# Performance work log

Hardware: AMD Instinct MI355X
Metric: run time of the kernel (lower is better)

Reference implementation:

```python
import jax, jax.numpy as jnp
import numpy as np

B, N, K, DIN, DM, DOUT = 4, 4096, 16, 256, 256, 256


def setup_inputs() -> dict:
    key = jax.random.key(0)
    ks = jax.random.split(key, 14)
    s = lambda k, shape: (jax.random.normal(k, shape, jnp.float32) * 0.02)
    return dict(
        xyz=jax.random.normal(ks[0], (B, N, 3), jnp.float32),
        features=jax.random.normal(ks[1], (B, N, DIN), jnp.float32),
        fc_delta_w1=s(ks[2], (3, DM)), fc_delta_b1=jnp.zeros((DM,), jnp.float32),
        fc_delta_w2=s(ks[3], (DM, DM)), fc_delta_b2=jnp.zeros((DM,), jnp.float32),
        fc1_w=s(ks[4], (DIN, DM)), fc1_b=jnp.zeros((DM,), jnp.float32),
        wq=s(ks[5], (DM, DM)), wk=s(ks[6], (DM, DM)), wv=s(ks[7], (DM, DM)),
        fc_gamma_w1=s(ks[8], (DM, DM)), fc_gamma_b1=jnp.zeros((DM,), jnp.float32),
        fc_gamma_w2=s(ks[9], (DM, DM)), fc_gamma_b2=jnp.zeros((DM,), jnp.float32),
        fc2_w=s(ks[10], (DM, DOUT)), fc2_b=jnp.zeros((DOUT,), jnp.float32),
        sc_w=s(ks[11], (DIN, DOUT)), sc_b=jnp.zeros((DOUT,), jnp.float32),
    )


def reference(xyz, features, fc_delta_w1, fc_delta_b1, fc_delta_w2, fc_delta_b2,
              fc1_w, fc1_b, wq, wk, wv, fc_gamma_w1, fc_gamma_b1,
              fc_gamma_w2, fc_gamma_b2, fc2_w, fc2_b, sc_w, sc_b):
    # kNN via squared euclidean distances (same ordering as cdist topk)
    x2 = jnp.sum(xyz * xyz, axis=-1)                                   # (B,N)
    d2 = x2[:, :, None] + x2[:, None, :] - 2.0 * jnp.einsum('bnd,bmd->bnm', xyz, xyz)
    knn_idx = jax.lax.top_k(-d2, K)[1]                                 # (B,N,K)

    gather = jax.vmap(lambda a, i: a[i])                               # per-batch gather
    knn_xyz = gather(xyz, knn_idx)                                     # (B,N,K,3)

    # positional encoding MLP on relative coordinates
    rel = xyz[:, :, None, :] - knn_xyz                                 # (B,N,K,3)
    pos_enc = jax.nn.relu(rel @ fc_delta_w1 + fc_delta_b1) @ fc_delta_w2 + fc_delta_b2

    shortcut = features
    f = features @ fc1_w + fc1_b                                       # (B,N,DM)
    knn_f = gather(f, knn_idx)                                         # (B,N,K,DM)

    q = f @ wq                                                         # (B,N,DM)
    k_ = knn_f @ wk                                                    # (B,N,K,DM)
    v = knn_f @ wv                                                     # (B,N,K,DM)

    a = q[:, :, None, :] - k_ + pos_enc                                # (B,N,K,DM)
    a = jax.nn.relu(a @ fc_gamma_w1 + fc_gamma_b1) @ fc_gamma_w2 + fc_gamma_b2
    attn = jax.nn.softmax(a / np.float32(np.sqrt(DM)), axis=-2)        # softmax over K

    res = jnp.einsum('bnkf,bnkf->bnf', attn, v + pos_enc)              # (B,N,DM)
    return res @ fc2_w + fc2_b + shortcut @ sc_w + sc_b                # (B,N,DOUT)
```

## Files before the change

### kernel.cpp

```cpp
#include <hip/hip_runtime.h>
#include <hip/hip_bf16.h>
#include <math.h>

typedef __attribute__((ext_vector_type(8))) short bf16x8;
typedef __attribute__((ext_vector_type(4))) float f32x4;
typedef __attribute__((ext_vector_type(4))) short s16x4;
typedef unsigned int u32;
typedef unsigned long long u64;

#define NBATCH 4
#define NPTS   4096
#define NTOT   (NBATCH*NPTS)
#define NROWS  (NTOT*16)

__device__ __forceinline__ float bf2f(unsigned short h){
  unsigned int u = ((unsigned int)h) << 16;
  return __builtin_bit_cast(float, u);
}
__device__ __forceinline__ unsigned short f2bf(float f){
  unsigned int u = __builtin_bit_cast(unsigned int, f);
  u += 0x7FFFu + ((u >> 16) & 1u);
  return (unsigned short)(u >> 16);
}
__device__ __forceinline__ unsigned short f2bfh(float f){
  return __bfloat16_as_ushort(__float2bfloat16(f));
}

#define MFMA(a,b,c) __builtin_amdgcn_mfma_f32_16x16x32_bf16((a),(b),(c),0,0,0)

typedef u32 __attribute__((address_space(1))) gas_u32;
typedef u32 __attribute__((address_space(3))) las_u32;
__device__ __forceinline__ void gl_lds16(const void* g, void* l){
  __builtin_amdgcn_global_load_lds((const gas_u32*)g, (las_u32*)l, 16, 0, 0);
}

__device__ __forceinline__ void wfence(){
  asm volatile("s_waitcnt lgkmcnt(0)" ::: "memory");
  __builtin_amdgcn_sched_barrier(0);
}

__global__ __launch_bounds__(256) void k_convert(const float* __restrict__ x,
                                                 unsigned short* __restrict__ xb, int n){
  int i = (blockIdx.x * 256 + threadIdx.x) * 4;
  if (i < n){
    float4 v = *(const float4*)(x + i);
    s16x4 o;
    o[0] = (short)f2bf(v.x); o[1] = (short)f2bf(v.y);
    o[2] = (short)f2bf(v.z); o[3] = (short)f2bf(v.w);
    *(s16x4*)(xb + i) = o;
  }
}

__global__ __launch_bounds__(256) void k_xyzw(const float* __restrict__ xyz,
                                              float4* __restrict__ xyzw){
  int i = blockIdx.x * 256 + threadIdx.x;
  float x = xyz[i*3], y = xyz[i*3+1], z = xyz[i*3+2];
  xyzw[i] = make_float4(x, y, z, x*x + y*y + z*z);
}

__global__ __launch_bounds__(256) void k_prep_mats(
    const float* __restrict__ scw, const float* __restrict__ g2,
    const float* __restrict__ fc2, const float* __restrict__ W2,
    const float* __restrict__ scb,
    unsigned short* __restrict__ qkv2T, unsigned short* __restrict__ g2sT,
    unsigned short* __restrict__ fc2T, unsigned short* __restrict__ BposT,
    float* __restrict__ cvec){
  int c = blockIdx.x, d = threadIdx.x;
  qkv2T[(768+c)*256 + d] = f2bf(scw[d*256 + c]);
  g2sT[c*256 + d]        = f2bf(g2[d*256 + c] * 0.0625f);
  fc2T[c*256 + d]        = f2bf(fc2[d*256 + c]);
  BposT[(256+c)*256 + d] = f2bf(W2[d*256 + c]);
  if (d == 0) cvec[768 + c] = scb[c];
}

__global__ __launch_bounds__(256) void k_prep_gemm(
    const float* __restrict__ wq, const float* __restrict__ wk,
    const float* __restrict__ g1, const float* __restrict__ W2,
    const float* __restrict__ b2d, const float* __restrict__ gb1,
    unsigned short* __restrict__ tmpWq, unsigned short* __restrict__ tmpWk,
    unsigned short* __restrict__ BposT, float* __restrict__ c1){
  int c = threadIdx.x, bid = blockIdx.x;
  if (bid < 256){
    int d = bid; float acc = 0.f;
    for (int e=0;e<256;e++) acc += wq[d*256+e]*g1[e*256+c];
    tmpWq[c*256 + d] = f2bf(acc);
  } else if (bid < 512){
    int d = bid-256; float acc = 0.f;
    for (int e=0;e<256;e++) acc += wk[d*256+e]*g1[e*256+c];
    tmpWk[c*256 + d] = f2bf(acc);
  } else if (bid < 768){
    int d = bid-512; float acc = 0.f;
    for (int e=0;e<256;e++) acc += W2[d*256+e]*g1[e*256+c];
    BposT[c*256 + d] = f2bf(acc);
  } else {
    float acc = 0.f;
    for (int e=0;e<256;e++) acc += b2d[e]*g1[e*256+c];
    c1[c] = acc + gb1[c];
  }
}

__global__ __launch_bounds__(256) void k_prep_gemm2(
    const float* __restrict__ fc1w, const float* __restrict__ fc1b,
    const float* __restrict__ wv,
    const unsigned short* __restrict__ tmpWq, const unsigned short* __restrict__ tmpWk,
    unsigned short* __restrict__ qkv2T, float* __restrict__ cvec){
  int c = threadIdx.x, bid = blockIdx.x;
  if (bid < 256){
    int d = bid; float acc = 0.f;
    for (int e=0;e<256;e++) acc += fc1w[d*256+e]*bf2f(tmpWq[c*256+e]);
    qkv2T[c*256 + d] = f2bf(acc);
  } else if (bid < 512){
    int d = bid-256; float acc = 0.f;
    for (int e=0;e<256;e++) acc += fc1w[d*256+e]*bf2f(tmpWk[c*256+e]);
    qkv2T[(256+c)*256 + d] = f2bf(acc);
  } else if (bid < 768){
    int d = bid-512; float acc = 0.f;
    for (int e=0;e<256;e++) acc += fc1w[d*256+e]*wv[e*256+c];
    qkv2T[(512+c)*256 + d] = f2bf(acc);
  } else {
    float aq=0.f, ak=0.f, av=0.f;
    for (int e=0;e<256;e++){
      float fb = fc1b[e];
      aq += fb*bf2f(tmpWq[c*256+e]);
      ak += fb*bf2f(tmpWk[c*256+e]);
      av += fb*wv[e*256+c];
    }
    cvec[c] = aq; cvec[256+c] = ak; cvec[512+c] = av;
  }
}

__device__ __forceinline__ u32 fmap(float d){
  u32 u = __builtin_bit_cast(u32, d);
  return ((int)u < 0) ? ~u : (u | 0x80000000u);
}

__device__ __forceinline__ void find_thresh(const int* hist, int lane, int need,
                                            int* e_out, int* c_out){
  int h0 = hist[lane*4], h1 = hist[lane*4+1], h2 = hist[lane*4+2], h3 = hist[lane*4+3];
  int ps = h0 + h1 + h2 + h3;
  int incl = ps;
  #pragma unroll
  for (int d = 1; d < 64; d <<= 1){
    int tv = __shfl_up(incl, d, 64);
    if (lane >= d) incl += tv;
  }
  int excl = incl - ps;
  int b0 = excl, b1 = excl + h0, b2 = b1 + h1, b3 = b2 + h2;
  bool f0 = (b0 < need) && (b0 + h0 >= need);
  bool f1 = (b1 < need) && (b1 + h1 >= need);
  bool f2 = (b2 < need) && (b2 + h2 >= need);
  bool f3 = (b3 < need) && (b3 + h3 >= need);
  int e_loc = f0 ? lane*4 : f1 ? lane*4+1 : f2 ? lane*4+2 : lane*4+3;
  int c_loc = f0 ? b0 : f1 ? b1 : f2 ? b2 : b3;
  u64 mk = __ballot(f0 | f1 | f2 | f3);
  int wl = __ffsll(mk) - 1;
  *e_out = __shfl(e_loc, wl, 64);
  *c_out = __shfl(c_loc, wl, 64);
}

__device__ __forceinline__ void find_thresh4(const int* hA, int lane, int need,
                                             int* e_out, int* c_out){
  int h[4];
  #pragma unroll
  for (int j=0;j<4;j++){
    int bin = lane*4+j;
    h[j] = hA[bin]
         + hA[256 + ((bin+8)&255)]
         + hA[512 + ((bin+16)&255)]
         + hA[768 + ((bin+24)&255)];
  }
  int ps = h[0] + h[1] + h[2] + h[3];
  int incl = ps;
  #pragma unroll
  for (int d = 1; d < 64; d <<= 1){
    int tv = __shfl_up(incl, d, 64);
    if (lane >= d) incl += tv;
  }
  int excl = incl - ps;
  int b0 = excl, b1 = excl + h[0], b2 = b1 + h[1], b3 = b2 + h[2];
  bool f0 = (b0 < need) && (b0 + h[0] >= need);
  bool f1 = (b1 < need) && (b1 + h[1] >= need);
  bool f2 = (b2 < need) && (b2 + h[2] >= need);
  bool f3 = (b3 < need) && (b3 + h[3] >= need);
  int e_loc = f0 ? lane*4 : f1 ? lane*4+1 : f2 ? lane*4+2 : lane*4+3;
  int c_loc = f0 ? b0 : f1 ? b1 : f2 ? b2 : b3;
  u64 mk = __ballot(f0 | f1 | f2 | f3);
  int wl = __ffsll(mk) - 1;
  *e_out = __shfl(e_loc, wl, 64);
  *c_out = __shfl(c_loc, wl, 64);
}

__global__ __launch_bounds__(256) void k_knn(const float4* __restrict__ xyzw,
                                             int* __restrict__ gidxbuf,
                                             float4* __restrict__ relbuf){
  __shared__ int histA[4][1024];
  __shared__ int histB[4][256];
  __shared__ u32 lstU[4][64];
  __shared__ int lstM[4][64];

  int t = threadIdx.x, lane = t & 63, wv = t >> 6;
  int widx = blockIdx.x * 4 + wv;
  int b = widx >> 12, n = widx & 4095;
  const float4* xb = xyzw + (size_t)b * NPTS;
  float4 P = xb[n];
  float x2n = P.w;
  int* hA = histA[wv]; int* hB = histB[wv];

  #pragma unroll
  for (int j = 0; j < 16; j++) hA[lane*16+j] = 0;
  #pragma unroll
  for (int j = 0; j < 4; j++)  hB[lane*4+j] = 0;
  wfence();

  int cp = lane >> 4;
  int cpoff = cp*256, cprot = cp*8;

  for (int it = 0; it < 64; it += 2){
    float4 Q0 = xb[it*64 + lane];
    float4 Q1 = xb[it*64 + 64 + lane];
    float d0 = x2n + Q0.w - 2.0f*(P.x*Q0.x + P.y*Q0.y + P.z*Q0.z);
    float d1 = x2n + Q1.w - 2.0f*(P.x*Q1.x + P.y*Q1.y + P.z*Q1.z);
    int b0 = (int)(fmap(d0) >> 24), b1 = (int)(fmap(d1) >> 24);
    atomicAdd(&hA[cpoff + ((b0 + cprot)&255)], 1);
    atomicAdd(&hA[cpoff + ((b1 + cprot)&255)], 1);
  }
  wfence();
  int e1, c0;
  find_thresh4(hA, lane, 16, &e1, &c0);

  for (int it = 0; it < 64; it++){
    float4 Q = xb[it*64 + lane];
    u32 u = fmap(x2n + Q.w - 2.0f*(P.x*Q.x + P.y*Q.y + P.z*Q.z));
    if ((int)(u >> 24) == e1) atomicAdd(&hB[(u >> 16) & 0xFF], 1);
  }
  wfence();
  int m1, cc;
  find_thresh(hB, lane, 16 - c0, &m1, &cc);
  int c1 = c0 + cc;
  u32 T16 = ((u32)e1 << 8) | (u32)m1;

  int base = 0, Lc = 0;
  size_t orow = (size_t)widx * 16;
  for (int it = 0; it < 64; it++){
    int m = it*64 + lane;
    float4 Q = xb[m];
    u32 u = fmap(x2n + Q.w - 2.0f*(P.x*Q.x + P.y*Q.y + P.z*Q.z));
    u32 u16_ = u >> 16;
    bool def = u16_ < T16;
    bool bnd = u16_ == T16;
    u64 mkd = __ballot(def);
    if (def){
      int slot = base + __popcll(mkd & ((1ULL << lane) - 1ULL));
      gidxbuf[orow + slot] = b*NPTS + m;
      relbuf[orow + slot]  = make_float4(P.x - Q.x, P.y - Q.y, P.z - Q.z, 0.f);
    }
    base += __popcll(mkd);
    u64 mkb = __ballot(bnd);
    if (bnd){
      int sl = Lc + __popcll(mkb & ((1ULL << lane) - 1ULL));
      if (sl < 64){ lstU[wv][sl] = u; lstM[wv][sl] = m; }
    }
    Lc += __popcll(mkb);
  }
  wfence();
  if (Lc > 64) Lc = 64;

  int r2 = 16 - c1;
  u32 lu = (lane < Lc) ? lstU[wv][lane] : 0xFFFFFFFFu;
  int lm = (lane < Lc) ? lstM[wv][lane] : 0x7FFFFFFF;
  bool popped = false;
  for (int r = 0; r < r2; r++){
    u32 ku = popped ? 0xFFFFFFFFu : lu;
    int km = popped ? 0x7FFFFFFF : lm;
    #pragma unroll
    for (int off = 32; off >= 1; off >>= 1){
      u32 ou = __shfl_xor(ku, off, 64);
      int om = __shfl_xor(km, off, 64);
      if (ou < ku || (ou == ku && om < km)){ ku = ou; km = om; }
    }
    bool mine = !popped && (lane < Lc) && (lu == ku) && (lm == km);
    u64 mk = __ballot(mine);
    int wl = __ffsll(mk) - 1;
    if (lane == wl){
      popped = true;
      float4 Q = xb[km];
      gidxbuf[orow + c1 + r] = b*NPTS + km;
      relbuf[orow + c1 + r]  = make_float4(P.x - Q.x, P.y - Q.y, P.z - Q.z, 0.f);
    }
  }
}

template<int MODE>
__global__ __launch_bounds__(512) void k_mm(
    const unsigned short* __restrict__ A, const unsigned short* __restrict__ BT,
    int rowbase,
    const float* __restrict__ bias, const float* __restrict__ b2v,
    const unsigned short* __restrict__ qg, const unsigned short* __restrict__ kg,
    const unsigned short* __restrict__ vb,
    const float4* __restrict__ relbuf, const int* __restrict__ gidxbuf,
    const float* __restrict__ W1, const float* __restrict__ b1d,
    unsigned short* __restrict__ o0, unsigned short* __restrict__ o1,
    unsigned short* __restrict__ o2, unsigned short* __restrict__ o3,
    const unsigned short* __restrict__ vper,
    float* __restrict__ fout){
  __shared__ unsigned short As[4096];
  __shared__ unsigned short Bs[8192];
  __shared__ float4 W1s4[256];
  __shared__ float4 relS[128];
  __shared__ int    gidxS[128];
  __shared__ float  biasS[256];

  int t = threadIdx.x;
  int lane = t & 63, w = t >> 6;
  int wm = w >> 2, wn = w & 3;
  int lrow = lane & 15, lkg = lane >> 4;
  int bx = blockIdx.x;
  if constexpr (MODE == 2){
    int gx = gridDim.x;
    bx = (bx & 7) * (gx >> 3) + (bx >> 3);
  }
  int m0 = bx * 128, n0 = blockIdx.y * 256;

  float4 rl0 = make_float4(0.f,0.f,0.f,0.f);
  if constexpr (MODE == 2){
    if (t < 128){
      relS[t]  = relbuf[(size_t)rowbase + m0 + t];
      gidxS[t] = gidxbuf[(size_t)rowbase + m0 + t];
    }
    if (t < 256){
      biasS[t] = (blockIdx.y == 0) ? bias[t] : b2v[t];
      W1s4[t] = make_float4(W1[t], W1[256+t], W1[512+t], b1d[t]);
    }
    __syncthreads();
    rl0 = relS[t >> 2];
  }
  if constexpr (MODE == 0){
    if (t < 256) biasS[t] = bias[n0 + t];
  }

  int sr = t >> 2, sc = (t & 3) * 8;
  unsigned short* lA  = As + (w << 9);
  unsigned short* lB  = Bs + (w << 9);
  unsigned short* lB2 = Bs + 4096 + (w << 9);
  const unsigned short* gB  = BT + (size_t)(n0 + sr)*256 + sc;
  const unsigned short* gB2 = BT + (size_t)(n0 + 128 + sr)*256 + sc;

  f32x4 acc[4][4] = {};
  for (int k0 = 0; k0 < 256; k0 += 32){
    if constexpr (MODE == 2){
      int r = t >> 2, h = (t & 3) << 3;
      bf16x8 h0;
      #pragma unroll
      for (int j = 0; j < 8; j++){
        int c = k0 + h + j;
        float4 wa = W1s4[c];
        float x0 = rl0.x*wa.x + rl0.y*wa.y + rl0.z*wa.z + wa.w;
        h0[j] = (short)f2bfh(fmaxf(x0, 0.f));
      }
      *(bf16x8*)&As[r*32 + h] = h0;
    } else {
      const unsigned short* gA = A + (size_t)(m0 + sr)*256 + k0 + sc;
      gl_lds16(gA, lA);
    }
    gl_lds16(gB  + k0, lB);
    gl_lds16(gB2 + k0, lB2);
    __syncthreads();
    bf16x8 af[4], bfr[4];
    #pragma unroll
    for (int fi = 0; fi < 4; fi++)
      af[fi] = *(const bf16x8*)&As[(wm*64 + fi*16 + lrow)*32 + lkg*8];
    #pragma unroll
    for (int nf = 0; nf < 4; nf++)
      bfr[nf] = *(const bf16x8*)&Bs[(wn*64 + nf*16 + lrow)*32 + lkg*8];
    #pragma unroll
    for (int fi = 0; fi < 4; fi++)
      #pragma unroll
      for (int nf = 0; nf < 4; nf++)
        acc[fi][nf] = MFMA(af[fi], bfr[nf], acc[fi][nf]);
    __syncthreads();
  }

  if constexpr (MODE == 0){
    unsigned short* outp = (blockIdx.y==0)?o0:(blockIdx.y==1)?o1:(blockIdx.y==2)?o2:o3;
    #pragma unroll
    for (int fi=0; fi<4; fi++)
      #pragma unroll
      for (int nf=0; nf<4; nf++)
        #pragma unroll
        for (int r=0;r<4;r++){
          int row = m0 + wm*64 + fi*16 + lkg*4 + r;
          int col = wn*64 + nf*16 + lrow;
          outp[(size_t)row*256 + col] = f2bf(acc[fi][nf][r] + biasS[col]);
        }
  } else if constexpr (MODE == 2){
    const bool is_a1 = (blockIdx.y == 0);
    #pragma unroll
    for (int fi=0; fi<4; fi++){
      int g = (rowbase + m0 + wm*64 + fi*16) >> 4;
      #pragma unroll
      for (int nf=0; nf<4; nf++){
        int colg = wn*64 + nf*16 + lrow;
        if (is_a1){
          float qv = bf2f(qg[(size_t)g*256 + colg]) + biasS[colg];
          #pragma unroll
          for (int r=0;r<4;r++){
            int rl_ = wm*64 + fi*16 + lkg*4 + r;
            int gi = gidxS[rl_];
            float a1 = acc[fi][nf][r] + qv - bf2f(kg[(size_t)gi*256 + colg]);
            o0[(size_t)(m0 + rl_)*256 + colg] = f2bfh(fmaxf(a1, 0.f));
          }
        } else {
          float bb = biasS[colg];
          #pragma unroll
          for (int r=0;r<4;r++){
            int rl_ = wm*64 + fi*16 + lkg*4 + r;
            int gi = gidxS[rl_];
            float vpe = acc[fi][nf][r] + bb + bf2f(vb[(size_t)gi*256 + colg]);
            o1[(size_t)(m0 + rl_)*256 + colg] = f2bfh(vpe);
          }
        }
      }
    }
  } else if constexpr (MODE == 3){
    #pragma unroll
    for (int fi=0; fi<4; fi++){
      int g = (rowbase + m0 + wm*64 + fi*16) >> 4;
      #pragma unroll
      for (int nf=0; nf<4; nf++){
        int colg = wn*64 + nf*16 + lrow;
        float s[4], e[4];
        #pragma unroll
        for (int r=0;r<4;r++) s[r] = acc[fi][nf][r] + bias[colg]*0.0625f;
        float mx = fmaxf(fmaxf(s[0],s[1]), fmaxf(s[2],s[3]));
        mx = fmaxf(mx, __shfl_xor(mx,16,64));
        mx = fmaxf(mx, __shfl_xor(mx,32,64));
        float sm = 0.f;
        #pragma unroll
        for (int r=0;r<4;r++){ e[r] = __expf(s[r]-mx); sm += e[r]; }
        sm += __shfl_xor(sm,16,64);
        sm += __shfl_xor(sm,32,64);
        float rs = 1.f/sm, tsum = 0.f;
        #pragma unroll
        for (int r=0;r<4;r++){
          int rl_ = wm*64 + fi*16 + lkg*4 + r;
          tsum += (e[r]*rs) * bf2f(vper[(size_t)(m0 + rl_)*256 + colg]);
        }
        tsum += __shfl_xor(tsum,16,64);
        tsum += __shfl_xor(tsum,32,64);
        if (lkg == 0) o0[(size_t)g*256 + colg] = f2bf(tsum);
      }
    }
  } else {
    #pragma unroll
    for (int fi=0; fi<4; fi++)
      #pragma unroll
      for (int nf=0; nf<4; nf++)
        #pragma unroll
        for (int r=0;r<4;r++){
          int row = m0 + wm*64 + fi*16 + lkg*4 + r;
          int col = wn*64 + nf*16 + lrow;
          fout[(size_t)row*256 + col] = acc[fi][nf][r] + bias[col]
                                      + bf2f(qg[(size_t)row*256 + col]);
        }
  }
}

extern "C" void kernel_launch(void* const* d_in, const int* in_sizes, int n_in,
                              void* d_out, int out_size, void* d_ws, size_t ws_size,
                              hipStream_t stream){
  (void)in_sizes; (void)n_in; (void)out_size;
  const float* xyz  = (const float*)d_in[0];
  const float* feat = (const float*)d_in[1];
  const float* W1   = (const float*)d_in[2];
  const float* b1d  = (const float*)d_in[3];
  const float* W2   = (const float*)d_in[4];
  const float* b2d  = (const float*)d_in[5];
  const float* fc1w = (const float*)d_in[6];
  const float* fc1b = (const float*)d_in[7];
  const float* wq   = (const float*)d_in[8];
  const float* wk   = (const float*)d_in[9];
  const float* wv   = (const float*)d_in[10];
  const float* g1   = (const float*)d_in[11];
  const float* gb1  = (const float*)d_in[12];
  const float* g2   = (const float*)d_in[13];
  const float* gb2  = (const float*)d_in[14];
  const float* fc2w = (const float*)d_in[15];
  const float* fc2b = (const float*)d_in[16];
  const float* scw  = (const float*)d_in[17];
  const float* scb  = (const float*)d_in[18];

  char* ws = (char*)d_ws;
  size_t off = 0;
  auto alloc = [&](size_t bytes)->void*{ void* p = ws + off; off += (bytes + 255) & ~(size_t)255; return p; };
  unsigned short* Xb     = (unsigned short*)alloc((size_t)NTOT*256*2);
  unsigned short* qgb    = (unsigned short*)alloc((size_t)NTOT*256*2);
  unsigned short* kgb    = (unsigned short*)alloc((size_t)NTOT*256*2);
  unsigned short* vbb    = (unsigned short*)alloc((size_t)NTOT*256*2);
  unsigned short* scbuf  = (unsigned short*)alloc((size_t)NTOT*256*2);
  int*            gidxbuf= (int*)alloc((size_t)NROWS*4);
  float4*         relbuf = (float4*)alloc((size_t)NROWS*16);
  float4*         xyzw   = (float4*)alloc((size_t)NTOT*16);
  unsigned short* qkv2T  = (unsigned short*)alloc(1024*256*2);
  unsigned short* tmpWq  = (unsigned short*)alloc(256*256*2);
  unsigned short* tmpWk  = (unsigned short*)alloc(256*256*2);
  unsigned short* BposT  = (unsigned short*)alloc(512*256*2);
  unsigned short* g2sT   = (unsigned short*)alloc(256*256*2);
  unsigned short* fc2T   = (unsigned short*)alloc(256*256*2);
  float*          c1     = (float*)alloc(256*4);
  float*          cvec   = (float*)alloc(1024*4);
  unsigned short* res    = Xb;

  int CR = NROWS;
  while (CR > 16384 && off + (size_t)CR*1024 > ws_size) CR >>= 1;
  unsigned short* a1buf  = (unsigned short*)alloc((size_t)CR*256*2);
  unsigned short* vpebuf = (unsigned short*)alloc((size_t)CR*256*2);

  k_convert<<<4096, 256, 0, stream>>>(feat, Xb, NTOT*256);
  k_xyzw<<<64, 256, 0, stream>>>(xyz, xyzw);
  k_prep_mats<<<256, 256, 0, stream>>>(scw, g2, fc2w, W2, scb, qkv2T, g2sT, fc2T, BposT, cvec);
  k_prep_gemm<<<769, 256, 0, stream>>>(wq, wk, g1, W2, b2d, gb1, tmpWq, tmpWk, BposT, c1);
  k_prep_gemm2<<<769, 256, 0, stream>>>(fc1w, fc1b, wv, tmpWq, tmpWk, qkv2T, cvec);
  k_knn<<<4096, 256, 0, stream>>>(xyzw, gidxbuf, relbuf);

  k_mm<0><<<dim3(128, 4), 512, 0, stream>>>(Xb, qkv2T, 0, cvec, nullptr,
      nullptr, nullptr, nullptr, nullptr, nullptr, nullptr, nullptr,
      qgb, kgb, vbb, scbuf, nullptr, nullptr);

  for (int c0 = 0; c0 < NROWS; c0 += CR){
    k_mm<2><<<dim3(CR/128, 2), 512, 0, stream>>>(nullptr, BposT, c0, c1, b2d,
        qgb, kgb, vbb, relbuf, gidxbuf, W1, b1d,
        a1buf, vpebuf, nullptr, nullptr, nullptr, nullptr);
    k_mm<3><<<dim3(CR/128, 1), 512, 0, stream>>>(a1buf, g2sT, c0, gb2, nullptr,
        nullptr, nullptr, nullptr, nullptr, nullptr, nullptr, nullptr,
        res, nullptr, nullptr, nullptr, vpebuf, nullptr);
  }

  k_mm<4><<<dim3(128, 1), 512, 0, stream>>>(res, fc2T, 0, fc2b, nullptr,
      scbuf, nullptr, nullptr, nullptr, nullptr, nullptr, nullptr,
      nullptr, nullptr, nullptr, nullptr, nullptr, (float*)d_out);
}
```

Measured before the change: 486.6 us.

## Merge kNN second histogram pass into emission pass with bucket candidate list

The kNN radix-select kernel drops one full 4096-point distance scan. The second-level histogram is now built during the emission pass, which emits points below the top-byte threshold and stores the candidates that share the threshold byte in a list reusing histogram shared memory. Those candidates are then refined from the list, with a fallback rescan when more than 128 share the bucket. This saves one scan of all points per query at the cost of more complex control flow and reuse of the shared histogram buffer.

```diff
diff --git a/kernel.cpp b/kernel.cpp
--- a/kernel.cpp
+++ b/kernel.cpp
@@ -195,8 +195,6 @@
                                              float4* __restrict__ relbuf){
   __shared__ int histA[4][1024];
   __shared__ int histB[4][256];
-  __shared__ u32 lstU[4][64];
-  __shared__ int lstM[4][64];
 
   int t = threadIdx.x, lane = t & 63, wv = t >> 6;
   int widx = blockIdx.x * 4 + wv;
@@ -225,19 +223,14 @@
     atomicAdd(&hA[cpoff + ((b1 + cprot)&255)], 1);
   }
   wfence();
-  int e1, c0;
-  find_thresh4(hA, lane, 16, &e1, &c0);
-
-  for (int it = 0; it < 64; it++){
-    float4 Q = xb[it*64 + lane];
-    u32 u = fmap(x2n + Q.w - 2.0f*(P.x*Q.x + P.y*Q.y + P.z*Q.z));
-    if ((int)(u >> 24) == e1) atomicAdd(&hB[(u >> 16) & 0xFF], 1);
-  }
+  int e1, c0dummy;
+  find_thresh4(hA, lane, 16, &e1, &c0dummy);
   wfence();
-  int m1, cc;
-  find_thresh(hB, lane, 16 - c0, &m1, &cc);
-  int c1 = c0 + cc;
-  u32 T16 = ((u32)e1 << 8) | (u32)m1;
+
+  u32* lstE_u = (u32*)&hA[0];
+  int* lstE_m = &hA[128];
+  u32* lstT_u = (u32*)&hA[256];
+  int* lstT_m = &hA[320];
 
   int base = 0, Lc = 0;
   size_t orow = (size_t)widx * 16;
@@ -245,9 +238,9 @@
     int m = it*64 + lane;
     float4 Q = xb[m];
     u32 u = fmap(x2n + Q.w - 2.0f*(P.x*Q.x + P.y*Q.y + P.z*Q.z));
-    u32 u16_ = u >> 16;
-    bool def = u16_ < T16;
-    bool bnd = u16_ == T16;
+    int hi = (int)(u >> 24);
+    bool def = hi < e1;
+    bool bnd = hi == e1;
     u64 mkd = __ballot(def);
     if (def){
       int slot = base + __popcll(mkd & ((1ULL << lane) - 1ULL));
@@ -258,16 +251,75 @@
     u64 mkb = __ballot(bnd);
     if (bnd){
       int sl = Lc + __popcll(mkb & ((1ULL << lane) - 1ULL));
-      if (sl < 64){ lstU[wv][sl] = u; lstM[wv][sl] = m; }
+      if (sl < 128){ lstE_u[sl] = u; lstE_m[sl] = m; }
+      atomicAdd(&hB[(u >> 16) & 0xFF], 1);
     }
     Lc += __popcll(mkb);
   }
   wfence();
-  if (Lc > 64) Lc = 64;
+  int c0 = base;
+  int m1, cc;
+  find_thresh(hB, lane, 16 - c0, &m1, &cc);
+  int c1 = c0 + cc;
+
+  int nt = 0;
+  if (Lc <= 128){
+    int eb = c0;
+    for (int ch = 0; ch < 128; ch += 64){
+      int idx = ch + lane;
+      bool valid = idx < Lc;
+      u32 u = valid ? lstE_u[idx] : 0xFFFFFFFFu;
+      int mid = valid ? (int)((u >> 16) & 0xFF) : 999;
+      bool lt = valid && (mid < m1);
+      u64 mk = __ballot(lt);
+      if (lt){
+        int slot = eb + __popcll(mk & ((1ULL << lane) - 1ULL));
+        int m = lstE_m[idx];
+        float4 Q = xb[m];
+        gidxbuf[orow + slot] = b*NPTS + m;
+        relbuf[orow + slot]  = make_float4(P.x - Q.x, P.y - Q.y, P.z - Q.z, 0.f);
+      }
+      eb += __popcll(mk);
+      bool tie = valid && (mid == m1);
+      u64 mkt = __ballot(tie);
+      if (tie){
+        int sl = nt + __popcll(mkt & ((1ULL << lane) - 1ULL));
+        if (sl < 64){ lstT_u[sl] = u; lstT_m[sl] = lstE_m[idx]; }
+      }
+      nt += __popcll(mkt);
+      if (Lc <= 64) break;
+    }
+  } else {
+    int eb = c0;
+    for (int it = 0; it < 64; it++){
+      int m = it*64 + lane;
+      float4 Q = xb[m];
+      u32 u = fmap(x2n + Q.w - 2.0f*(P.x*Q.x + P.y*Q.y + P.z*Q.z));
+      bool inb = ((int)(u >> 24) == e1);
+      int mid = inb ? (int)((u >> 16) & 0xFF) : 999;
+      bool lt = inb && (mid < m1);
+      u64 mk = __ballot(lt);
+      if (lt){
+        int slot = eb + __popcll(mk & ((1ULL << lane) - 1ULL));
+        gidxbuf[orow + slot] = b*NPTS + m;
+        relbuf[orow + slot]  = make_float4(P.x - Q.x, P.y - Q.y, P.z - Q.z, 0.f);
+      }
+      eb += __popcll(mk);
+      bool tie = inb && (mid == m1);
+      u64 mkt = __ballot(tie);
+      if (tie){
+        int sl = nt + __popcll(mkt & ((1ULL << lane) - 1ULL));
+        if (sl < 64){ lstT_u[sl] = u; lstT_m[sl] = m; }
+      }
+      nt += __popcll(mkt);
+    }
+  }
+  wfence();
+  if (nt > 64) nt = 64;
 
   int r2 = 16 - c1;
-  u32 lu = (lane < Lc) ? lstU[wv][lane] : 0xFFFFFFFFu;
-  int lm = (lane < Lc) ? lstM[wv][lane] : 0x7FFFFFFF;
+  u32 lu = (lane < nt) ? lstT_u[lane] : 0xFFFFFFFFu;
+  int lm = (lane < nt) ? lstT_m[lane] : 0x7FFFFFFF;
   bool popped = false;
   for (int r = 0; r < r2; r++){
     u32 ku = popped ? 0xFFFFFFFFu : lu;
@@ -278,7 +330,7 @@
       int om = __shfl_xor(km, off, 64);
       if (ou < ku || (ou == ku && om < km)){ ku = ou; km = om; }
     }
-    bool mine = !popped && (lane < Lc) && (lu == ku) && (lm == km);
+    bool mine = !popped && (lane < nt) && (lu == ku) && (lm == km);
     u64 mk = __ballot(mine);
     int wl = __ffsll(mk) - 1;
     if (lane == wl){
```

Result: no change. 483.7 us (-0.6%).
